# Kernel optimization log

Hardware: AMD Instinct MI355X
Metric: run time of the kernel (lower is better)

Reference implementation:

```python
import jax, jax.numpy as jnp
import numpy as np

B, Hh, Ww, C = 64, 14, 14, 2048   # batch, feat map H, W, encoder_dim
E, D, A, V, L = 512, 512, 512, 30000, 32  # embed, decoder, attn dims, vocab, max text len
SC = 0.02


def setup_inputs() -> dict:
    key = jax.random.key(0)
    ks = jax.random.split(key, 16)
    def p(k, shape):
        return jax.random.normal(k, shape, jnp.float32) * SC
    lens = jax.random.randint(ks[2], (B, 1), 2, L + 1).at[0, 0].set(L)  # ensure max len present -> static T
    return {
        "encoder_out": jax.random.normal(ks[0], (B, Hh, Ww, C), jnp.float32),
        "encoded_text": jax.random.randint(ks[1], (B, L), 0, V),
        "encoded_text_len": lens,
        "W_init_h": p(ks[3], (C, D)), "b_init_h": jnp.zeros((D,), jnp.float32),
        "W_init_c": p(ks[4], (C, D)), "b_init_c": jnp.zeros((D,), jnp.float32),
        "W_en": p(ks[5], (C, A)), "b_en": jnp.zeros((A,), jnp.float32),
        "W_de": p(ks[6], (D, A)), "b_de": jnp.zeros((A,), jnp.float32),
        "W_at": p(ks[7], (A, 1)), "b_at": jnp.zeros((1,), jnp.float32),
        "W_gate": p(ks[8], (D, C)), "b_gate": jnp.zeros((C,), jnp.float32),
        "W_ih": p(ks[9], (C + E, 4 * D)), "b_ih": jnp.zeros((4 * D,), jnp.float32),
        "W_hh": p(ks[10], (D, 4 * D)), "b_hh": jnp.zeros((4 * D,), jnp.float32),
        "embed_table": p(ks[11], (V, E)),
        "W_head": p(ks[12], (D, V)), "b_head": jnp.zeros((V,), jnp.float32),
    }


def reference(encoder_out, encoded_text, encoded_text_len,
              W_init_h, b_init_h, W_init_c, b_init_c,
              W_en, b_en, W_de, b_de, W_at, b_at,
              W_gate, b_gate, W_ih, b_ih, W_hh, b_hh,
              embed_table, W_head, b_head):
    b, hh, ww, c = encoder_out.shape
    img = encoder_out.reshape(b, hh * ww, c)          # [b, p, c]
    img_mean = img.mean(axis=1)
    # NOTE: original computes h0/c0 on UNSORTED img and never reindexes them (repo quirk); reproduced faithfully.
    h0 = img_mean @ W_init_h + b_init_h               # [b, d]
    c0 = img_mean @ W_init_c + b_init_c
    tl = encoded_text_len[:, 0]
    idx = jnp.argsort(-tl, stable=True)               # descending stable sort
    img_s = img[idx]
    text_s = encoded_text[idx]
    tlen = tl[idx] - 1                                # decode steps per example
    T = encoded_text.shape[1] - 1                     # static: one row has full length L
    emb = embed_table[text_s[:, :T]]                  # [b, T, e]
    en_attn = img_s @ W_en + b_en                     # [b, p, a] time-invariant attn projection

    def step(carry, xs):
        h, cst = carry
        emb_t, mask = xs                              # [b,e], [b]
        de = h @ W_de + b_de                          # [b, a]
        score = (jax.nn.relu(en_attn + de[:, None, :]) @ W_at)[..., 0] + b_at[0]  # [b, p]
        alpha = jax.nn.softmax(score, axis=1)
        ctx = jnp.einsum('bp,bpc->bc', alpha, img_s)
        gate = jax.nn.sigmoid(h @ W_gate + b_gate)
        x = jnp.concatenate([ctx * gate, emb_t], axis=1)
        gates = x @ W_ih + b_ih + h @ W_hh + b_hh     # [b, 4d], torch LSTMCell gate order i,f,g,o
        i, f, g, o = jnp.split(gates, 4, axis=1)
        c_new = jax.nn.sigmoid(f) * cst + jax.nn.sigmoid(i) * jnp.tanh(g)
        h_new = jax.nn.sigmoid(o) * jnp.tanh(c_new)
        m = mask[:, None]
        h = jnp.where(m, h_new, h)
        cst = jnp.where(m, c_new, cst)
        pred = jnp.where(m, h_new @ W_head + b_head, 0.0)  # dropout in eval mode = identity
        attn = jnp.where(m, alpha, 0.0)
        return (h, cst), (pred, attn)

    emb_T = jnp.swapaxes(emb, 0, 1)                   # [T, b, e]
    masks = jnp.arange(T)[:, None] < tlen[None, :]    # [T, b] prefix-active (lengths sorted desc)
    (_, _), (preds, attns) = jax.lax.scan(step, (h0, c0), (emb_T, masks))
    prediction = jnp.swapaxes(preds, 0, 1)            # [b, T, V]
    attention = jnp.swapaxes(attns, 0, 1)             # [b, T, p]
    return prediction, text_s, tlen, attention, idx
```

## Files before the change

### kernel.cpp

```cpp
#include <hip/hip_runtime.h>
#include <hip/hip_bf16.h>
#include <math.h>

#define BB 64
#define PP 196
#define CC 2048
#define DD 512
#define AA 512
#define EE 512
#define VV 30000
#define VPAD 30016
#define LL 32
#define TT 31
#define XH 2560
#define HEADBLK 469

typedef short bf16x8 __attribute__((ext_vector_type(8)));
typedef float f32x4 __attribute__((ext_vector_type(4)));

__device__ inline unsigned short f2bf(float x) {
    __hip_bfloat16 h = __float2bfloat16(x);
    return __builtin_bit_cast(unsigned short, h);
}
__device__ inline float bf2f(unsigned short u) {
    unsigned int x = ((unsigned int)u) << 16;
    return __builtin_bit_cast(float, x);
}

template<int NA, int K, int LDA>
__device__ inline void mmN(const unsigned short* __restrict__ a0,
                           const unsigned short* __restrict__ b0,
                           f32x4 acc[4]) {
#pragma unroll
    for (int kc = 0; kc < K / 32; ++kc) {
        bf16x8 bfr = *reinterpret_cast<const bf16x8*>(b0 + kc * 32);
#pragma unroll
        for (int mt = 0; mt < NA; ++mt) {
            bf16x8 afr = *reinterpret_cast<const bf16x8*>(a0 + (size_t)mt * 16 * LDA + kc * 32);
            acc[mt] = __builtin_amdgcn_mfma_f32_16x16x32_bf16(afr, bfr, acc[mt], 0, 0, 0);
        }
    }
}

template<int K, int LDA>
__device__ inline void mmD(int nAct, const unsigned short* __restrict__ a0,
                           const unsigned short* __restrict__ b0, f32x4 acc[4]) {
    switch (nAct) {
        case 4: mmN<4, K, LDA>(a0, b0, acc); break;
        case 3: mmN<3, K, LDA>(a0, b0, acc); break;
        case 2: mmN<2, K, LDA>(a0, b0, acc); break;
        case 1: mmN<1, K, LDA>(a0, b0, acc); break;
        default: break;
    }
}


__global__ void k_sort(const int* __restrict__ text, const int* __restrict__ lens,
                       int* __restrict__ idx, int* __restrict__ inv, int* __restrict__ tlen,
                       int* __restrict__ ts,
                       float* __restrict__ out_text, float* __restrict__ out_tlen,
                       float* __restrict__ out_idx) {
    int j = threadIdx.x;
    __shared__ int key[BB];
    __shared__ int sidx[BB];
    key[j] = lens[j];
    __syncthreads();
    int kj = key[j];
    int pos = 0;
    for (int q = 0; q < BB; ++q) {
        int kq = key[q];
        if (kq > kj || (kq == kj && q < j)) pos++;
    }
    sidx[pos] = j;
    __syncthreads();
    int src = sidx[j];
    idx[j] = src;
    inv[src] = j;
    int tl = key[src] - 1;
    tlen[j] = tl;
    out_idx[j] = (float)src;
    out_tlen[j] = (float)tl;
    for (int l = 0; l < LL; ++l) {
        int tok = text[src * LL + l];
        ts[j * LL + l] = tok;
        out_text[j * LL + l] = (float)tok;
    }
}

__global__ __launch_bounds__(256) void k_cvtenc(const float* __restrict__ enc, const int* __restrict__ idx,
                                                unsigned short* __restrict__ enc_bf) {
    int row = blockIdx.x;
    int bs = row / PP, p = row - bs * PP;
    int c0 = threadIdx.x * 8;
    const float* src = enc + ((size_t)idx[bs] * PP + p) * CC + c0;
    f32x4 lo = *reinterpret_cast<const f32x4*>(src);
    f32x4 hi = *reinterpret_cast<const f32x4*>(src + 4);
    unsigned short* dst = enc_bf + (size_t)row * CC + c0;
    bf16x8 v;
    v[0] = (short)f2bf(lo[0]); v[1] = (short)f2bf(lo[1]);
    v[2] = (short)f2bf(lo[2]); v[3] = (short)f2bf(lo[3]);
    v[4] = (short)f2bf(hi[0]); v[5] = (short)f2bf(hi[1]);
    v[6] = (short)f2bf(hi[2]); v[7] = (short)f2bf(hi[3]);
    *reinterpret_cast<bf16x8*>(dst) = v;
}

__global__ __launch_bounds__(256) void k_meanbf(const unsigned short* __restrict__ enc_bf,
                                                const int* __restrict__ inv,
                                                unsigned short* __restrict__ mean_bf) {
    int b = blockIdx.x;
    int lane = threadIdx.x & 31, pg = threadIdx.x >> 5;
    int c0 = blockIdx.y * 256 + lane * 8;
    const unsigned short* img = enc_bf + (size_t)inv[b] * PP * CC + c0;
    float s[8] = {0.f, 0.f, 0.f, 0.f, 0.f, 0.f, 0.f, 0.f};
    for (int p = pg; p < PP; p += 8) {
        bf16x8 v = *reinterpret_cast<const bf16x8*>(img + (size_t)p * CC);
#pragma unroll
        for (int j = 0; j < 8; ++j) s[j] += bf2f((unsigned short)v[j]);
    }
    __shared__ float red[8][256];
#pragma unroll
    for (int j = 0; j < 8; ++j) red[pg][lane * 8 + j] = s[j];
    __syncthreads();
    int c = threadIdx.x;
    float tt = 0.f;
#pragma unroll
    for (int g = 0; g < 8; ++g) tt += red[g][c];
    mean_bf[(size_t)b * CC + blockIdx.y * 256 + c] = f2bf(tt * (1.0f / PP));
}

__global__ __launch_bounds__(64) void k_init_mfma(const unsigned short* __restrict__ mean_bf,
                                                  const unsigned short* __restrict__ Wt_ih,
                                                  const unsigned short* __restrict__ Wt_ic,
                                                  const float* __restrict__ bh, const float* __restrict__ bc,
                                                  unsigned short* __restrict__ xh_bf, float* __restrict__ c_f32) {
    int isC = blockIdx.x >= 32;
    int n0 = (blockIdx.x & 31) * 16;
    int lane = threadIdx.x;
    const unsigned short* Wt = isC ? Wt_ic : Wt_ih;
    const unsigned short* a0 = mean_bf + (size_t)(lane & 15) * CC + ((lane >> 4) * 8);
    const unsigned short* b0 = Wt + (size_t)(n0 + (lane & 15)) * CC + ((lane >> 4) * 8);
    f32x4 acc[4];
#pragma unroll
    for (int mt = 0; mt < 4; ++mt) acc[mt] = (f32x4){0.f, 0.f, 0.f, 0.f};
    mmN<4, CC, CC>(a0, b0, acc);
    int n = n0 + (lane & 15);
    float bv = (isC ? bc : bh)[n];
#pragma unroll
    for (int mt = 0; mt < 4; ++mt)
#pragma unroll
        for (int r = 0; r < 4; ++r) {
            int m = mt * 16 + (lane >> 4) * 4 + r;
            float val = acc[mt][r] + bv;
            if (isC) c_f32[(size_t)m * DD + n] = val;
            else     xh_bf[(size_t)m * XH + CC + n] = f2bf(val);
        }
}

__global__ __launch_bounds__(256) void k_transcvt(const float* __restrict__ src, int K, int N,
                                                  unsigned short* __restrict__ dst, int dstStride, int Npad) {
    __shared__ float t[32][33];
    int n0 = blockIdx.x * 32, k0 = blockIdx.y * 32;
    int tx = threadIdx.x, ty = threadIdx.y;
#pragma unroll
    for (int r = 0; r < 4; ++r) {
        int k = k0 + ty + r * 8;
        int n = n0 + tx;
        t[ty + r * 8][tx] = (n < N) ? src[(size_t)k * N + n] : 0.f;
    }
    __syncthreads();
#pragma unroll
    for (int r = 0; r < 4; ++r) {
        int n = n0 + ty + r * 8;
        int k = k0 + tx;
        if (n < Npad) dst[(size_t)n * dstStride + k] = f2bf(t[tx][ty + r * 8]);
    }
}

__global__ __launch_bounds__(256) void k_emball(const float* __restrict__ embed, const int* __restrict__ ts,
                                                unsigned short* __restrict__ emb_all) {
    int row = blockIdx.x;
    int t = row >> 6, b = row & 63;
    int tok = ts[b * LL + t];
    int e = threadIdx.x * 2;
    const float* src = embed + (size_t)tok * EE + e;
    unsigned short* dst = emb_all + (size_t)row * EE + e;
    dst[0] = f2bf(src[0]);
    dst[1] = f2bf(src[1]);
}

__global__ __launch_bounds__(256) void k_embw(const unsigned short* __restrict__ emb_all,
                                              const unsigned short* __restrict__ Wt_emb,
                                              const float* __restrict__ bih, const float* __restrict__ bhh,
                                              float* __restrict__ embW) {
    int tstep = blockIdx.x;
    int n0 = blockIdx.y * 64;
    int lane = threadIdx.x & 63, w = threadIdx.x >> 6;
    const unsigned short* a0 = emb_all + ((size_t)tstep * 64 + (lane & 15)) * EE + ((lane >> 4) * 8);
    const unsigned short* b0 = Wt_emb + (size_t)(n0 + w * 16 + (lane & 15)) * EE + ((lane >> 4) * 8);
    f32x4 acc[4];
#pragma unroll
    for (int mt = 0; mt < 4; ++mt) acc[mt] = (f32x4){0.f, 0.f, 0.f, 0.f};
    mmN<4, EE, EE>(a0, b0, acc);
    int n = n0 + w * 16 + (lane & 15);
    float bv = bih[n] + bhh[n];
#pragma unroll
    for (int mt = 0; mt < 4; ++mt)
#pragma unroll
        for (int r = 0; r < 4; ++r) {
            int m = mt * 16 + (lane >> 4) * 4 + r;
            embW[((size_t)tstep * 64 + m) * 2048 + n] = acc[mt][r] + bv;
        }
}

__global__ __launch_bounds__(256) void k_enattn_mfma(const unsigned short* __restrict__ enc_bf,
                                                     const unsigned short* __restrict__ Wt,
                                                     const float* __restrict__ bias,
                                                     unsigned short* __restrict__ en_bf) {
    int m0 = blockIdx.x * 64;
    int lane = threadIdx.x & 63, w = threadIdx.x >> 6;
    const unsigned short* a0 = enc_bf + (size_t)(m0 + (lane & 15)) * CC + ((lane >> 4) * 8);
    const unsigned short* bptr[8];
#pragma unroll
    for (int nt = 0; nt < 8; ++nt) {
        int rowB = nt * 64 + w * 16 + (lane & 15);
        bptr[nt] = Wt + (size_t)rowB * CC + ((lane >> 4) * 8);
    }
    f32x4 acc[4][8];
#pragma unroll
    for (int mt = 0; mt < 4; ++mt)
#pragma unroll
        for (int nt = 0; nt < 8; ++nt) acc[mt][nt] = (f32x4){0.f, 0.f, 0.f, 0.f};

    for (int kc = 0; kc < CC / 32; ++kc) {
        bf16x8 afr[4];
#pragma unroll
        for (int mt = 0; mt < 4; ++mt)
            afr[mt] = *reinterpret_cast<const bf16x8*>(a0 + (size_t)mt * 16 * CC + kc * 32);
#pragma unroll
        for (int nt = 0; nt < 8; ++nt) {
            bf16x8 bfr = *reinterpret_cast<const bf16x8*>(bptr[nt] + kc * 32);
#pragma unroll
            for (int mt = 0; mt < 4; ++mt)
                acc[mt][nt] = __builtin_amdgcn_mfma_f32_16x16x32_bf16(afr[mt], bfr, acc[mt][nt], 0, 0, 0);
        }
    }
#pragma unroll
    for (int nt = 0; nt < 8; ++nt) {
        int n = nt * 64 + w * 16 + (lane & 15);
        float bv = bias[n];
#pragma unroll
        for (int mt = 0; mt < 4; ++mt)
#pragma unroll
            for (int r = 0; r < 4; ++r) {
                int m = m0 + mt * 16 + (lane >> 4) * 4 + r;
                en_bf[(size_t)m * AA + n] = f2bf(acc[mt][nt][r] + bv);
            }
    }
}

__global__ __launch_bounds__(256) void k_pre0(const unsigned short* __restrict__ xh_bf,
                                              const unsigned short* __restrict__ Wt_de,
                                              const float* __restrict__ b_de,
                                              const unsigned short* __restrict__ Wt_gate,
                                              const float* __restrict__ b_gate,
                                              float* __restrict__ de, float* __restrict__ gsig) {
    int lane = threadIdx.x & 63, w = threadIdx.x >> 6;
    int l15 = lane & 15, hi = lane >> 4;
    const unsigned short* a0 = xh_bf + CC + (size_t)l15 * XH + hi * 8;
    f32x4 acc[4];
#pragma unroll
    for (int mt = 0; mt < 4; ++mt) acc[mt] = (f32x4){0.f, 0.f, 0.f, 0.f};
    if (blockIdx.x < 8) {
        int n0 = (blockIdx.x * 4 + w) * 16;
        const unsigned short* b0 = Wt_de + (size_t)(n0 + l15) * DD + hi * 8;
        mmN<4, DD, XH>(a0, b0, acc);
        int n = n0 + l15;
        float bv = b_de[n];
#pragma unroll
        for (int mt = 0; mt < 4; ++mt)
#pragma unroll
            for (int r = 0; r < 4; ++r) {
                int m = mt * 16 + hi * 4 + r;
                de[(size_t)m * AA + n] = acc[mt][r] + bv;
            }
    } else {
        int n0 = (blockIdx.x - 8) * 64 + w * 16;
        const unsigned short* b0 = Wt_gate + (size_t)(n0 + l15) * DD + hi * 8;
        mmN<4, DD, XH>(a0, b0, acc);
        int n = n0 + l15;
        float bv = b_gate[n];
#pragma unroll
        for (int mt = 0; mt < 4; ++mt)
#pragma unroll
            for (int r = 0; r < 4; ++r) {
                int m = mt * 16 + hi * 4 + r;
                gsig[(size_t)m * CC + n] = 1.f / (1.f + expf(-(acc[mt][r] + bv)));
            }
    }
}


__global__ __launch_bounds__(256) void k_score(const unsigned short* __restrict__ en_bf,
                                               const float* __restrict__ de,
                                               const float* __restrict__ Wat, const float* __restrict__ bat,
                                               const int* __restrict__ tlen, int t,
                                               float* __restrict__ alpha, float* __restrict__ out_attn) {
    int b = blockIdx.x;
    int tid = threadIdx.x;
    if (t >= tlen[b]) {
        if (tid < PP) out_attn[((size_t)b * TT + t) * PP + tid] = 0.f;
        return;
    }
    __shared__ float deL[AA];
    __shared__ float watL[AA];
    __shared__ float red[256];
    deL[tid] = de[(size_t)b * AA + tid];
    deL[tid + 256] = de[(size_t)b * AA + 256 + tid];
    watL[tid] = Wat[tid];
    watL[tid + 256] = Wat[tid + 256];
    __syncthreads();
    float s0 = 0.f, s1 = 0.f;
    if (tid < PP) {
        const unsigned short* er = en_bf + ((size_t)b * PP + tid) * AA;
#pragma unroll 2
        for (int a16 = 0; a16 < AA / 16; ++a16) {
            bf16x8 v0 = *reinterpret_cast<const bf16x8*>(er + a16 * 16);
            bf16x8 v1 = *reinterpret_cast<const bf16x8*>(er + a16 * 16 + 8);
#pragma unroll
            for (int j = 0; j < 8; ++j) {
                float u0 = fmaxf(bf2f((unsigned short)v0[j]) + deL[a16 * 16 + j], 0.f);
                float u1 = fmaxf(bf2f((unsigned short)v1[j]) + deL[a16 * 16 + 8 + j], 0.f);
                s0 = fmaf(u0, watL[a16 * 16 + j], s0);
                s1 = fmaf(u1, watL[a16 * 16 + 8 + j], s1);
            }
        }
    }
    float s = s0 + s1 + bat[0];
    red[tid] = (tid < PP) ? s : -3.4e38f;
    __syncthreads();
    for (int st = 128; st > 0; st >>= 1) {
        if (tid < st) red[tid] = fmaxf(red[tid], red[tid + st]);
        __syncthreads();
    }
    float m = red[0];
    __syncthreads();
    float e = (tid < PP) ? expf(s - m) : 0.f;
    red[tid] = e;
    __syncthreads();
    for (int st = 128; st > 0; st >>= 1) {
        if (tid < st) red[tid] += red[tid + st];
        __syncthreads();
    }
    float inv = 1.0f / red[0];
    if (tid < PP) {
        float al = e * inv;
        alpha[(size_t)b * PP + tid] = al;
        out_attn[((size_t)b * TT + t) * PP + tid] = al;
    }
}

__global__ __launch_bounds__(256) void k_ctxg(const unsigned short* __restrict__ enc_bf,
                                              const float* __restrict__ alpha,
                                              const float* __restrict__ gsig,
                                              const int* __restrict__ tlen, int t,
                                              unsigned short* __restrict__ xh_bf) {
    int b = blockIdx.x;
    if (t >= tlen[b]) return;
    int lane = threadIdx.x & 31, pg = threadIdx.x >> 5;
    int c0 = blockIdx.y * 256 + lane * 8;
    __shared__ float al[PP];
    if (threadIdx.x < PP) al[threadIdx.x] = alpha[(size_t)b * PP + threadIdx.x];
    __syncthreads();
    const unsigned short* img = enc_bf + (size_t)b * PP * CC + c0;
    float s[8] = {0.f, 0.f, 0.f, 0.f, 0.f, 0.f, 0.f, 0.f};
    for (int p = pg; p < PP; p += 8) {
        float a = al[p];
        bf16x8 v = *reinterpret_cast<const bf16x8*>(img + (size_t)p * CC);
#pragma unroll
        for (int j = 0; j < 8; ++j) s[j] = fmaf(a, bf2f((unsigned short)v[j]), s[j]);
    }
    __shared__ float red[8][256];
#pragma unroll
    for (int j = 0; j < 8; ++j) red[pg][lane * 8 + j] = s[j];
    __syncthreads();
    int c = blockIdx.y * 256 + threadIdx.x;
    float tt = 0.f;
#pragma unroll
    for (int g = 0; g < 8; ++g) tt += red[g][threadIdx.x];
    xh_bf[(size_t)b * XH + c] = f2bf(tt * gsig[(size_t)b * CC + c]);
}

__global__ __launch_bounds__(256) void k_gateslstm(const unsigned short* __restrict__ xh_bf,
                                                   const unsigned short* __restrict__ Wt,
                                                   const float* __restrict__ embW,
                                                   const int* __restrict__ tlen, int t,
                                                   unsigned short* __restrict__ xh_out,
                                                   float* __restrict__ c_f32,
                                                   unsigned short* __restrict__ hn_bf) {
    int nAct = (int)(t < tlen[0]) + (int)(t < tlen[16]) + (int)(t < tlen[32]) + (int)(t < tlen[48]);
    if (nAct == 0) return;
    int tid = threadIdx.x, wid = tid >> 6, lane = tid & 63;
    int col = lane & 15, hi = lane >> 4;
    int d0 = blockIdx.x * 16;
    const unsigned short* a0 = xh_bf + (size_t)col * XH + hi * 8;
    const unsigned short* b0 = Wt + (size_t)(wid * DD + d0 + col) * XH + hi * 8;

    f32x4 acc[4];
    const float* ew = embW + (size_t)t * 64 * 2048;
#pragma unroll
    for (int mt = 0; mt < 4; ++mt)
#pragma unroll
        for (int r = 0; r < 4; ++r) {
            int m = mt * 16 + hi * 4 + r;
            acc[mt][r] = ew[(size_t)m * 2048 + wid * DD + d0 + col];
        }
    mmD<XH, XH>(nAct, a0, b0, acc);

    __shared__ float lg[4][64][17];
#pragma unroll
    for (int mt = 0; mt < 4; ++mt)
#pragma unroll
        for (int r = 0; r < 4; ++r)
            lg[wid][mt * 16 + hi * 4 + r][col] = acc[mt][r];
    __syncthreads();

    if (wid < nAct) {
        int d = d0 + col;
#pragma unroll
        for (int r = 0; r < 4; ++r) {
            int b = wid * 16 + hi * 4 + r;
            float iv = lg[0][b][col], fv = lg[1][b][col], gv = lg[2][b][col], ov = lg[3][b][col];
            float cv = c_f32[(size_t)b * DD + d];
            float si = 1.f / (1.f + expf(-iv));
            float sf = 1.f / (1.f + expf(-fv));
            float so = 1.f / (1.f + expf(-ov));
            float cn = sf * cv + si * tanhf(gv);
            float hn = so * tanhf(cn);
            hn_bf[(size_t)b * DD + d] = f2bf(hn);
            if (t < tlen[b]) {
                xh_out[(size_t)b * XH + CC + d] = f2bf(hn);
                c_f32[(size_t)b * DD + d] = cn;
            }
        }
    }
}

__global__ __launch_bounds__(256) void k_head_de_gate(const unsigned short* __restrict__ hn_bf,
                                                      const unsigned short* __restrict__ Wt_head,
                                                      const float* __restrict__ b_head,
                                                      const unsigned short* __restrict__ xh_bf,
                                                      const unsigned short* __restrict__ Wt_de,
                                                      const float* __restrict__ b_de,
                                                      const unsigned short* __restrict__ Wt_gate,
                                                      const float* __restrict__ b_gate,
                                                      const int* __restrict__ tlen, int t,
                                                      float* __restrict__ out_pred,
                                                      float* __restrict__ de, float* __restrict__ gsig) {
    int lane = threadIdx.x & 63, w = threadIdx.x >> 6;
    int l15 = lane & 15, hi = lane >> 4;
    f32x4 acc[4];
#pragma unroll
    for (int mt = 0; mt < 4; ++mt) acc[mt] = (f32x4){0.f, 0.f, 0.f, 0.f};
    if (blockIdx.x < HEADBLK) {
        int nAct = (int)(t < tlen[0]) + (int)(t < tlen[16]) + (int)(t < tlen[32]) + (int)(t < tlen[48]);
        int n0 = blockIdx.x * 64;
        const unsigned short* a0 = hn_bf + (size_t)l15 * DD + hi * 8;
        const unsigned short* b0 = Wt_head + (size_t)(n0 + w * 16 + l15) * DD + hi * 8;
        mmD<DD, DD>(nAct, a0, b0, acc);
        int v = n0 + w * 16 + l15;
        if (v >= VV) return;
        float bv = b_head[v];
#pragma unroll
        for (int mt = 0; mt < 4; ++mt)
#pragma unroll
            for (int r = 0; r < 4; ++r) {
                int b = mt * 16 + hi * 4 + r;
                bool a = t < tlen[b];
                out_pred[(size_t)b * TT * VV + (size_t)t * VV + v] = a ? (acc[mt][r] + bv) : 0.f;
            }
    } else if (blockIdx.x < HEADBLK + 8) {
        int nAct = (int)(t + 1 < tlen[0]) + (int)(t + 1 < tlen[16]) + (int)(t + 1 < tlen[32]) + (int)(t + 1 < tlen[48]);
        int n0 = ((blockIdx.x - HEADBLK) * 4 + w) * 16;
        const unsigned short* a0 = xh_bf + CC + (size_t)l15 * XH + hi * 8;
        const unsigned short* b0 = Wt_de + (size_t)(n0 + l15) * DD + hi * 8;
        mmD<DD, XH>(nAct, a0, b0, acc);
        int n = n0 + l15;
        float bv = b_de[n];
#pragma unroll
        for (int mt = 0; mt < 4; ++mt)
#pragma unroll
            for (int r = 0; r < 4; ++r) {
                int m = mt * 16 + hi * 4 + r;
                de[(size_t)m * AA + n] = acc[mt][r] + bv;
            }
    } else {
        int nAct = (int)(t + 1 < tlen[0]) + (int)(t + 1 < tlen[16]) + (int)(t + 1 < tlen[32]) + (int)(t + 1 < tlen[48]);
        int n0 = (blockIdx.x - HEADBLK - 8) * 64 + w * 16;
        const unsigned short* a0 = xh_bf + CC + (size_t)l15 * XH + hi * 8;
        const unsigned short* b0 = Wt_gate + (size_t)(n0 + l15) * DD + hi * 8;
        mmD<DD, XH>(nAct, a0, b0, acc);
        int n = n0 + l15;
        float bv = b_gate[n];
#pragma unroll
        for (int mt = 0; mt < 4; ++mt)
#pragma unroll
            for (int r = 0; r < 4; ++r) {
                int m = mt * 16 + hi * 4 + r;
                gsig[(size_t)m * CC + n] = 1.f / (1.f + expf(-(acc[mt][r] + bv)));
            }
    }
}

extern "C" void kernel_launch(void* const* d_in, const int* in_sizes, int n_in,
                              void* d_out, int out_size, void* d_ws, size_t ws_size,
                              hipStream_t stream) {
    const float* enc     = (const float*)d_in[0];
    const int*   text    = (const int*)d_in[1];
    const int*   lens    = (const int*)d_in[2];
    const float* W_init_h = (const float*)d_in[3];
    const float* b_init_h = (const float*)d_in[4];
    const float* W_init_c = (const float*)d_in[5];
    const float* b_init_c = (const float*)d_in[6];
    const float* W_en    = (const float*)d_in[7];
    const float* b_en    = (const float*)d_in[8];
    const float* W_de    = (const float*)d_in[9];
    const float* b_de    = (const float*)d_in[10];
    const float* W_at    = (const float*)d_in[11];
    const float* b_at    = (const float*)d_in[12];
    const float* W_gate  = (const float*)d_in[13];
    const float* b_gate  = (const float*)d_in[14];
    const float* W_ih    = (const float*)d_in[15];
    const float* b_ih    = (const float*)d_in[16];
    const float* W_hh    = (const float*)d_in[17];
    const float* b_hh    = (const float*)d_in[18];
    const float* embed   = (const float*)d_in[19];
    const float* W_head  = (const float*)d_in[20];
    const float* b_head  = (const float*)d_in[21];

    float* outf = (float*)d_out;
    float* out_pred = outf;
    float* out_text = outf + (size_t)BB * TT * VV;
    float* out_tlen = out_text + BB * LL;
    float* out_attn = out_tlen + BB;
    float* out_idx  = out_attn + (size_t)BB * TT * PP;

    char* wsb = (char*)d_ws;
    int* idx  = (int*)wsb;
    int* inv  = idx + 64;
    int* tlen = inv + 64;
    int* ts   = tlen + 64;
    float* fw = (float*)(wsb + 16384);
    float* c_f32 = fw;  fw += (size_t)BB * DD;
    float* de    = fw;  fw += (size_t)BB * AA;
    float* alpha = fw;  fw += (size_t)BB * PP;
    float* gsig  = fw;  fw += (size_t)BB * CC;
    float* embW  = fw;  fw += (size_t)TT * BB * 2048;
    unsigned short* us = (unsigned short*)fw;
    unsigned short* mean_bf = us;  us += (size_t)BB * CC;
    unsigned short* xh_bf   = us;  us += (size_t)BB * XH;
    unsigned short* hn_bf   = us;  us += (size_t)BB * DD;
    unsigned short* emb_all = us;  us += (size_t)TT * BB * EE;
    unsigned short* en_bf   = us;  us += (size_t)BB * PP * AA;
    unsigned short* enc_bf  = us;  us += (size_t)BB * PP * CC;
    unsigned short* Wt_en   = us;  us += (size_t)AA * CC;
    unsigned short* Wt_de   = us;  us += (size_t)AA * DD;
    unsigned short* Wt_gate = us;  us += (size_t)CC * DD;
    unsigned short* Wt_emb  = us;  us += (size_t)2048 * EE;
    unsigned short* Wt_ihh  = us;  us += (size_t)2048 * XH;
    unsigned short* Wt_ih0  = us;  us += (size_t)DD * CC;
    unsigned short* Wt_ic0  = us;  us += (size_t)DD * CC;
    unsigned short* Wt_head = us;  us += (size_t)VPAD * DD;

    k_sort<<<1, 64, 0, stream>>>(text, lens, idx, inv, tlen, ts, out_text, out_tlen, out_idx);
    k_cvtenc<<<BB * PP, 256, 0, stream>>>(enc, idx, enc_bf);
    k_meanbf<<<dim3(BB, CC / 256), 256, 0, stream>>>(enc_bf, inv, mean_bf);

    dim3 tb(32, 8);
    k_transcvt<<<dim3(AA / 32, CC / 32), tb, 0, stream>>>(W_en, CC, AA, Wt_en, CC, AA);
    k_transcvt<<<dim3(AA / 32, DD / 32), tb, 0, stream>>>(W_de, DD, AA, Wt_de, DD, AA);
    k_transcvt<<<dim3(CC / 32, DD / 32), tb, 0, stream>>>(W_gate, DD, CC, Wt_gate, DD, CC);
    k_transcvt<<<dim3(CC / 32, CC / 32), tb, 0, stream>>>(W_ih, CC, 2048, Wt_ihh, XH, 2048);
    k_transcvt<<<dim3(CC / 32, DD / 32), tb, 0, stream>>>(W_hh, DD, 2048, Wt_ihh + CC, XH, 2048);
    k_transcvt<<<dim3(CC / 32, DD / 32), tb, 0, stream>>>(W_ih + (size_t)CC * 2048, DD, 2048, Wt_emb, EE, 2048);
    k_transcvt<<<dim3(DD / 32, CC / 32), tb, 0, stream>>>(W_init_h, CC, DD, Wt_ih0, CC, DD);
    k_transcvt<<<dim3(DD / 32, CC / 32), tb, 0, stream>>>(W_init_c, CC, DD, Wt_ic0, CC, DD);
    k_transcvt<<<dim3(VPAD / 32, DD / 32), tb, 0, stream>>>(W_head, DD, VV, Wt_head, DD, VPAD);

    k_init_mfma<<<64, 64, 0, stream>>>(mean_bf, Wt_ih0, Wt_ic0, b_init_h, b_init_c, xh_bf, c_f32);
    k_emball<<<TT * BB, 256, 0, stream>>>(embed, ts, emb_all);
    k_embw<<<dim3(TT, 2048 / 64), 256, 0, stream>>>(emb_all, Wt_emb, b_ih, b_hh, embW);
    k_enattn_mfma<<<PP, 256, 0, stream>>>(enc_bf, Wt_en, b_en, en_bf);
    k_pre0<<<40, 256, 0, stream>>>(xh_bf, Wt_de, b_de, Wt_gate, b_gate, de, gsig);

    for (int t = 0; t < TT; ++t) {
        k_score<<<BB, 256, 0, stream>>>(en_bf, de, W_at, b_at, tlen, t, alpha, out_attn);
        k_ctxg<<<dim3(BB, 8), 256, 0, stream>>>(enc_bf, alpha, gsig, tlen, t, xh_bf);
        k_gateslstm<<<DD / 16, 256, 0, stream>>>(xh_bf, Wt_ihh, embW, tlen, t, xh_bf, c_f32, hn_bf);
        k_head_de_gate<<<HEADBLK + 40, 256, 0, stream>>>(hn_bf, Wt_head, b_head, xh_bf, Wt_de, b_de,
                                                         Wt_gate, b_gate, tlen, t, out_pred, de, gsig);
    }
}
```

Measured before the change: 2.723 ms.

## Fuse attention score softmax and context gating into one kernel per step

Merges the score/softmax kernel and the context-weighted-sum kernel into a single 1024-thread block per batch item, keeping alpha in shared memory instead of a global buffer. This removes one kernel launch per decode step and the alpha round trip. In exchange, the context reduction now runs on only 64 blocks instead of 512, which reduces parallelism for the bandwidth-heavy encoder read.

```diff
diff --git a/kernel.cpp b/kernel.cpp
--- a/kernel.cpp
+++ b/kernel.cpp
@@ -300,52 +300,61 @@
 }
 
 
-__global__ __launch_bounds__(256) void k_score(const unsigned short* __restrict__ en_bf,
-                                               const float* __restrict__ de,
-                                               const float* __restrict__ Wat, const float* __restrict__ bat,
-                                               const int* __restrict__ tlen, int t,
-                                               float* __restrict__ alpha, float* __restrict__ out_attn) {
-    int b = blockIdx.x;
-    int tid = threadIdx.x;
+__global__ __launch_bounds__(1024) void k_attng(const unsigned short* __restrict__ en_bf,
+                                                const float* __restrict__ de,
+                                                const float* __restrict__ Wat, const float* __restrict__ bat,
+                                                const int* __restrict__ tlen, int t,
+                                                const unsigned short* __restrict__ enc_bf,
+                                                const float* __restrict__ gsig,
+                                                unsigned short* __restrict__ xh_bf,
+                                                float* __restrict__ out_attn) {
+    int b = blockIdx.x, tid = threadIdx.x;
     if (t >= tlen[b]) {
         if (tid < PP) out_attn[((size_t)b * TT + t) * PP + tid] = 0.f;
         return;
     }
     __shared__ float deL[AA];
     __shared__ float watL[AA];
+    __shared__ float sred[256][4];
+    __shared__ float sL[256];
     __shared__ float red[256];
-    deL[tid] = de[(size_t)b * AA + tid];
-    deL[tid + 256] = de[(size_t)b * AA + 256 + tid];
-    watL[tid] = Wat[tid];
-    watL[tid + 256] = Wat[tid + 256];
-    __syncthreads();
-    float s0 = 0.f, s1 = 0.f;
-    if (tid < PP) {
-        const unsigned short* er = en_bf + ((size_t)b * PP + tid) * AA;
-#pragma unroll 2
-        for (int a16 = 0; a16 < AA / 16; ++a16) {
-            bf16x8 v0 = *reinterpret_cast<const bf16x8*>(er + a16 * 16);
-            bf16x8 v1 = *reinterpret_cast<const bf16x8*>(er + a16 * 16 + 8);
+    __shared__ float red4[4][2048];
+    if (tid < 512) { deL[tid] = de[(size_t)b * AA + tid]; watL[tid] = Wat[tid]; }
+    __syncthreads();
+    int row = tid >> 2, ch = tid & 3;
+    float s = 0.f;
+    if (row < PP) {
+        const unsigned short* er = en_bf + ((size_t)b * PP + row) * AA + ch * 128;
+#pragma unroll
+        for (int a8 = 0; a8 < 16; ++a8) {
+            bf16x8 v = *reinterpret_cast<const bf16x8*>(er + a8 * 8);
 #pragma unroll
             for (int j = 0; j < 8; ++j) {
-                float u0 = fmaxf(bf2f((unsigned short)v0[j]) + deL[a16 * 16 + j], 0.f);
-                float u1 = fmaxf(bf2f((unsigned short)v1[j]) + deL[a16 * 16 + 8 + j], 0.f);
-                s0 = fmaf(u0, watL[a16 * 16 + j], s0);
-                s1 = fmaf(u1, watL[a16 * 16 + 8 + j], s1);
-            }
-        }
-    }
-    float s = s0 + s1 + bat[0];
-    red[tid] = (tid < PP) ? s : -3.4e38f;
+                int ix = ch * 128 + a8 * 8 + j;
+                float u = fmaxf(bf2f((unsigned short)v[j]) + deL[ix], 0.f);
+                s = fmaf(u, watL[ix], s);
+            }
+        }
+    }
+    sred[row][ch] = s;
+    __syncthreads();
+    float sc = 0.f;
+    if (tid < 256) {
+        sc = sred[tid][0] + sred[tid][1] + sred[tid][2] + sred[tid][3] + bat[0];
+        red[tid] = (tid < PP) ? sc : -3.4e38f;
+    }
     __syncthreads();
     for (int st = 128; st > 0; st >>= 1) {
         if (tid < st) red[tid] = fmaxf(red[tid], red[tid + st]);
         __syncthreads();
     }
-    float m = red[0];
-    __syncthreads();
-    float e = (tid < PP) ? expf(s - m) : 0.f;
-    red[tid] = e;
+    float mx = red[0];
+    __syncthreads();
+    if (tid < 256) {
+        float e = (tid < PP) ? expf(sc - mx) : 0.f;
+        sL[tid] = e;
+        red[tid] = e;
+    }
     __syncthreads();
     for (int st = 128; st > 0; st >>= 1) {
         if (tid < st) red[tid] += red[tid + st];
@@ -353,41 +362,28 @@
     }
     float inv = 1.0f / red[0];
     if (tid < PP) {
-        float al = e * inv;
-        alpha[(size_t)b * PP + tid] = al;
+        float al = sL[tid] * inv;
+        sL[tid] = al;
         out_attn[((size_t)b * TT + t) * PP + tid] = al;
     }
-}
-
-__global__ __launch_bounds__(256) void k_ctxg(const unsigned short* __restrict__ enc_bf,
-                                              const float* __restrict__ alpha,
-                                              const float* __restrict__ gsig,
-                                              const int* __restrict__ tlen, int t,
-                                              unsigned short* __restrict__ xh_bf) {
-    int b = blockIdx.x;
-    if (t >= tlen[b]) return;
-    int lane = threadIdx.x & 31, pg = threadIdx.x >> 5;
-    int c0 = blockIdx.y * 256 + lane * 8;
-    __shared__ float al[PP];
-    if (threadIdx.x < PP) al[threadIdx.x] = alpha[(size_t)b * PP + threadIdx.x];
-    __syncthreads();
+    __syncthreads();
+    int lane8 = tid & 255, pg = tid >> 8;
+    int c0 = lane8 * 8;
     const unsigned short* img = enc_bf + (size_t)b * PP * CC + c0;
-    float s[8] = {0.f, 0.f, 0.f, 0.f, 0.f, 0.f, 0.f, 0.f};
-    for (int p = pg; p < PP; p += 8) {
-        float a = al[p];
+    float s8[8] = {0.f, 0.f, 0.f, 0.f, 0.f, 0.f, 0.f, 0.f};
+    for (int p = pg; p < PP; p += 4) {
+        float a = sL[p];
         bf16x8 v = *reinterpret_cast<const bf16x8*>(img + (size_t)p * CC);
 #pragma unroll
-        for (int j = 0; j < 8; ++j) s[j] = fmaf(a, bf2f((unsigned short)v[j]), s[j]);
-    }
-    __shared__ float red[8][256];
-#pragma unroll
-    for (int j = 0; j < 8; ++j) red[pg][lane * 8 + j] = s[j];
-    __syncthreads();
-    int c = blockIdx.y * 256 + threadIdx.x;
-    float tt = 0.f;
-#pragma unroll
-    for (int g = 0; g < 8; ++g) tt += red[g][threadIdx.x];
-    xh_bf[(size_t)b * XH + c] = f2bf(tt * gsig[(size_t)b * CC + c]);
+        for (int j = 0; j < 8; ++j) s8[j] = fmaf(a, bf2f((unsigned short)v[j]), s8[j]);
+    }
+#pragma unroll
+    for (int j = 0; j < 8; ++j) red4[pg][c0 + j] = s8[j];
+    __syncthreads();
+    for (int c = tid; c < CC; c += 1024) {
+        float v = red4[0][c] + red4[1][c] + red4[2][c] + red4[3][c];
+        xh_bf[(size_t)b * XH + c] = f2bf(v * gsig[(size_t)b * CC + c]);
+    }
 }
 
 __global__ __launch_bounds__(256) void k_gateslstm(const unsigned short* __restrict__ xh_bf,
@@ -552,7 +548,6 @@
     float* fw = (float*)(wsb + 16384);
     float* c_f32 = fw;  fw += (size_t)BB * DD;
     float* de    = fw;  fw += (size_t)BB * AA;
-    float* alpha = fw;  fw += (size_t)BB * PP;
     float* gsig  = fw;  fw += (size_t)BB * CC;
     float* embW  = fw;  fw += (size_t)TT * BB * 2048;
     unsigned short* us = (unsigned short*)fw;
@@ -593,8 +588,7 @@
     k_pre0<<<40, 256, 0, stream>>>(xh_bf, Wt_de, b_de, Wt_gate, b_gate, de, gsig);
 
     for (int t = 0; t < TT; ++t) {
-        k_score<<<BB, 256, 0, stream>>>(en_bf, de, W_at, b_at, tlen, t, alpha, out_attn);
-        k_ctxg<<<dim3(BB, 8), 256, 0, stream>>>(enc_bf, alpha, gsig, tlen, t, xh_bf);
+        k_attng<<<BB, 1024, 0, stream>>>(en_bf, de, W_at, b_at, tlen, t, enc_bf, gsig, xh_bf, out_attn);
         k_gateslstm<<<DD / 16, 256, 0, stream>>>(xh_bf, Wt_ihh, embW, tlen, t, xh_bf, c_f32, hn_bf);
         k_head_de_gate<<<HEADBLK + 40, 256, 0, stream>>>(hn_bf, Wt_head, b_head, xh_bf, Wt_de, b_de,
                                                          Wt_gate, b_gate, tlen, t, out_pred, de, gsig);
```

Measured after the change: 2.932 ms. +7.7%, slower.

## Fuse attention score with context kernel and split LSTM gate GEMM over K

Applied to the files above, without the earlier changes.

Merges the attention score/softmax kernel into the context-gating kernel, so each of the 8 channel blocks per batch row recomputes the softmax locally. This removes the alpha buffer round-trip and one launch per decode step. The LSTM gates kernel now uses 512 threads, splitting the K dimension in half across two wave groups and summing the partials in shared memory. The fusion repeats the score computation 8 times per row, which adds reads of the projected encoder features.

```diff
diff --git a/kernel.cpp b/kernel.cpp
--- a/kernel.cpp
+++ b/kernel.cpp
@@ -300,20 +300,25 @@
 }
 
 
-__global__ __launch_bounds__(256) void k_score(const unsigned short* __restrict__ en_bf,
+__global__ __launch_bounds__(256) void k_actxg(const unsigned short* __restrict__ en_bf,
                                                const float* __restrict__ de,
                                                const float* __restrict__ Wat, const float* __restrict__ bat,
                                                const int* __restrict__ tlen, int t,
-                                               float* __restrict__ alpha, float* __restrict__ out_attn) {
+                                               const unsigned short* __restrict__ enc_bf,
+                                               const float* __restrict__ gsig,
+                                               unsigned short* __restrict__ xh_bf,
+                                               float* __restrict__ out_attn) {
     int b = blockIdx.x;
     int tid = threadIdx.x;
+    bool writer = (blockIdx.y == 0);
     if (t >= tlen[b]) {
-        if (tid < PP) out_attn[((size_t)b * TT + t) * PP + tid] = 0.f;
+        if (writer && tid < PP) out_attn[((size_t)b * TT + t) * PP + tid] = 0.f;
         return;
     }
     __shared__ float deL[AA];
     __shared__ float watL[AA];
     __shared__ float red[256];
+    __shared__ float al[PP];
     deL[tid] = de[(size_t)b * AA + tid];
     deL[tid + 256] = de[(size_t)b * AA + 256 + tid];
     watL[tid] = Wat[tid];
@@ -353,44 +358,33 @@
     }
     float inv = 1.0f / red[0];
     if (tid < PP) {
-        float al = e * inv;
-        alpha[(size_t)b * PP + tid] = al;
-        out_attn[((size_t)b * TT + t) * PP + tid] = al;
-    }
-}
-
-__global__ __launch_bounds__(256) void k_ctxg(const unsigned short* __restrict__ enc_bf,
-                                              const float* __restrict__ alpha,
-                                              const float* __restrict__ gsig,
-                                              const int* __restrict__ tlen, int t,
-                                              unsigned short* __restrict__ xh_bf) {
-    int b = blockIdx.x;
-    if (t >= tlen[b]) return;
-    int lane = threadIdx.x & 31, pg = threadIdx.x >> 5;
+        float a_ = e * inv;
+        al[tid] = a_;
+        if (writer) out_attn[((size_t)b * TT + t) * PP + tid] = a_;
+    }
+    __syncthreads();
+    int lane = tid & 31, pg = tid >> 5;
     int c0 = blockIdx.y * 256 + lane * 8;
-    __shared__ float al[PP];
-    if (threadIdx.x < PP) al[threadIdx.x] = alpha[(size_t)b * PP + threadIdx.x];
-    __syncthreads();
     const unsigned short* img = enc_bf + (size_t)b * PP * CC + c0;
-    float s[8] = {0.f, 0.f, 0.f, 0.f, 0.f, 0.f, 0.f, 0.f};
+    float sa[8] = {0.f, 0.f, 0.f, 0.f, 0.f, 0.f, 0.f, 0.f};
     for (int p = pg; p < PP; p += 8) {
         float a = al[p];
         bf16x8 v = *reinterpret_cast<const bf16x8*>(img + (size_t)p * CC);
 #pragma unroll
-        for (int j = 0; j < 8; ++j) s[j] = fmaf(a, bf2f((unsigned short)v[j]), s[j]);
-    }
-    __shared__ float red[8][256];
-#pragma unroll
-    for (int j = 0; j < 8; ++j) red[pg][lane * 8 + j] = s[j];
-    __syncthreads();
-    int c = blockIdx.y * 256 + threadIdx.x;
+        for (int j = 0; j < 8; ++j) sa[j] = fmaf(a, bf2f((unsigned short)v[j]), sa[j]);
+    }
+    __shared__ float r8[8][256];
+#pragma unroll
+    for (int j = 0; j < 8; ++j) r8[pg][lane * 8 + j] = sa[j];
+    __syncthreads();
+    int c = blockIdx.y * 256 + tid;
     float tt = 0.f;
 #pragma unroll
-    for (int g = 0; g < 8; ++g) tt += red[g][threadIdx.x];
+    for (int g = 0; g < 8; ++g) tt += r8[g][tid];
     xh_bf[(size_t)b * XH + c] = f2bf(tt * gsig[(size_t)b * CC + c]);
 }
 
-__global__ __launch_bounds__(256) void k_gateslstm(const unsigned short* __restrict__ xh_bf,
+__global__ __launch_bounds__(512) void k_gateslstm(const unsigned short* __restrict__ xh_bf,
                                                    const unsigned short* __restrict__ Wt,
                                                    const float* __restrict__ embW,
                                                    const int* __restrict__ tlen, int t,
@@ -400,23 +394,29 @@
     int nAct = (int)(t < tlen[0]) + (int)(t < tlen[16]) + (int)(t < tlen[32]) + (int)(t < tlen[48]);
     if (nAct == 0) return;
     int tid = threadIdx.x, wid = tid >> 6, lane = tid & 63;
+    int g = wid & 3, kh = wid >> 2;
     int col = lane & 15, hi = lane >> 4;
     int d0 = blockIdx.x * 16;
-    const unsigned short* a0 = xh_bf + (size_t)col * XH + hi * 8;
-    const unsigned short* b0 = Wt + (size_t)(wid * DD + d0 + col) * XH + hi * 8;
+    const unsigned short* a0 = xh_bf + (size_t)col * XH + kh * (XH / 2) + hi * 8;
+    const unsigned short* b0 = Wt + (size_t)(g * DD + d0 + col) * XH + kh * (XH / 2) + hi * 8;
 
     f32x4 acc[4];
-    const float* ew = embW + (size_t)t * 64 * 2048;
-#pragma unroll
-    for (int mt = 0; mt < 4; ++mt)
-#pragma unroll
-        for (int r = 0; r < 4; ++r) {
-            int m = mt * 16 + hi * 4 + r;
-            acc[mt][r] = ew[(size_t)m * 2048 + wid * DD + d0 + col];
-        }
-    mmD<XH, XH>(nAct, a0, b0, acc);
-
-    __shared__ float lg[4][64][17];
+    if (kh == 0) {
+        const float* ew = embW + (size_t)t * 64 * 2048;
+#pragma unroll
+        for (int mt = 0; mt < 4; ++mt)
+#pragma unroll
+            for (int r = 0; r < 4; ++r) {
+                int m = mt * 16 + hi * 4 + r;
+                acc[mt][r] = ew[(size_t)m * 2048 + g * DD + d0 + col];
+            }
+    } else {
+#pragma unroll
+        for (int mt = 0; mt < 4; ++mt) acc[mt] = (f32x4){0.f, 0.f, 0.f, 0.f};
+    }
+    mmD<XH / 2, XH>(nAct, a0, b0, acc);
+
+    __shared__ float lg[8][64][17];
 #pragma unroll
     for (int mt = 0; mt < 4; ++mt)
 #pragma unroll
@@ -429,7 +429,10 @@
 #pragma unroll
         for (int r = 0; r < 4; ++r) {
             int b = wid * 16 + hi * 4 + r;
-            float iv = lg[0][b][col], fv = lg[1][b][col], gv = lg[2][b][col], ov = lg[3][b][col];
+            float iv = lg[0][b][col] + lg[4][b][col];
+            float fv = lg[1][b][col] + lg[5][b][col];
+            float gv = lg[2][b][col] + lg[6][b][col];
+            float ov = lg[3][b][col] + lg[7][b][col];
             float cv = c_f32[(size_t)b * DD + d];
             float si = 1.f / (1.f + expf(-iv));
             float sf = 1.f / (1.f + expf(-fv));
@@ -552,7 +555,6 @@
     float* fw = (float*)(wsb + 16384);
     float* c_f32 = fw;  fw += (size_t)BB * DD;
     float* de    = fw;  fw += (size_t)BB * AA;
-    float* alpha = fw;  fw += (size_t)BB * PP;
     float* gsig  = fw;  fw += (size_t)BB * CC;
     float* embW  = fw;  fw += (size_t)TT * BB * 2048;
     unsigned short* us = (unsigned short*)fw;
@@ -593,9 +595,8 @@
     k_pre0<<<40, 256, 0, stream>>>(xh_bf, Wt_de, b_de, Wt_gate, b_gate, de, gsig);
 
     for (int t = 0; t < TT; ++t) {
-        k_score<<<BB, 256, 0, stream>>>(en_bf, de, W_at, b_at, tlen, t, alpha, out_attn);
-        k_ctxg<<<dim3(BB, 8), 256, 0, stream>>>(enc_bf, alpha, gsig, tlen, t, xh_bf);
-        k_gateslstm<<<DD / 16, 256, 0, stream>>>(xh_bf, Wt_ihh, embW, tlen, t, xh_bf, c_f32, hn_bf);
+        k_actxg<<<dim3(BB, 8), 256, 0, stream>>>(en_bf, de, W_at, b_at, tlen, t, enc_bf, gsig, xh_bf, out_attn);
+        k_gateslstm<<<DD / 16, 512, 0, stream>>>(xh_bf, Wt_ihh, embW, tlen, t, xh_bf, c_f32, hn_bf);
         k_head_de_gate<<<HEADBLK + 40, 256, 0, stream>>>(hn_bf, Wt_head, b_head, xh_bf, Wt_de, b_de,
                                                          Wt_gate, b_gate, tlen, t, out_pred, de, gsig);
     }
```

New measurement: 2.667 ms, median of 2. 1.02x faster.
